# Performance work log

Hardware: AMD Instinct MI355X
Metric: run time of the kernel (lower is better)

The kernel has to match this reference:

```python
import jax, jax.numpy as jnp
import numpy as np

EPS = 1e-12  # torch F.normalize eps

def _colnorm(w, g):
    # F.normalize(w, dim=0, p=2) * g  (column-wise L2 over dim 0)
    n = jnp.sqrt(jnp.sum(w * w, axis=0, keepdims=True))
    return (w / jnp.maximum(n, EPS)) * g

def setup_inputs() -> dict:
    key = jax.random.key(0)
    ks = jax.random.split(key, 16)
    B, T, V, E, H = 16, 512, 8192, 512, 1024
    inp = {
        'xs': jax.random.randint(ks[0], (B, T), 0, V),
        'ys': jax.random.randint(ks[1], (B, T), 0, V),
        'embed_w': jax.random.normal(ks[2], (V, E), jnp.float32) * 0.02,
        'wx': jax.random.normal(ks[3], (E, 4 * H), jnp.float32),
        'wh': jax.random.normal(ks[4], (H, 4 * H), jnp.float32),
        'wmx': jax.random.normal(ks[5], (E, H), jnp.float32),
        'wmh': jax.random.normal(ks[6], (H, H), jnp.float32),
        'b': jax.random.normal(ks[7], (4 * H,), jnp.float32) * 0.02,
        'gx': jax.random.normal(ks[8], (4 * H,), jnp.float32),
        'gh': jax.random.normal(ks[9], (4 * H,), jnp.float32),
        'gmx': jax.random.normal(ks[10], (H,), jnp.float32),
        'gmh': jax.random.normal(ks[11], (H,), jnp.float32),
        'pred_w': jax.random.normal(ks[12], (V, H), jnp.float32) * 0.02,
        'pred_b': jax.random.normal(ks[13], (V,), jnp.float32) * 0.02,
    }
    return inp

def reference(xs, ys, embed_w, wx, wh, wmx, wmh, b, gx, gh, gmx, gmh, pred_w, pred_b):
    B, T = xs.shape
    H = wmh.shape[0]
    V = pred_w.shape[0]
    # padding_idx=0 -> embedding row 0 is zero
    ew = embed_w.at[0].set(0.0)
    x = ew[xs]  # [B, T, E]
    # weight norm
    wx_n = _colnorm(wx, gx)
    wh_n = _colnorm(wh, gh)
    wmx_n = _colnorm(wmx, gmx)
    wmh_n = _colnorm(wmh, gmh)
    # precompute input-dependent projections (same math, batched over time)
    zx = jnp.einsum('bte,ef->btf', x, wx_n) + b     # [B, T, 4H]
    mx = jnp.einsum('bte,eh->bth', x, wmx_n)        # [B, T, H]

    def step(carry, inp):
        h, c = carry
        zx_t, mx_t = inp
        m = mx_t * (h @ wmh_n)                       # [B, H]
        z = zx_t + m @ wh_n                          # [B, 4H]
        i, f, o, u = jnp.split(z, 4, axis=1)
        i = jax.nn.sigmoid(i)
        f = jax.nn.sigmoid(f)
        o = jax.nn.sigmoid(o)
        u = jnp.tanh(u)
        c = f * c + i * u
        h = o * jnp.tanh(c)
        return (h, c), h

    h0 = jnp.zeros((B, H), x.dtype)
    c0 = jnp.zeros((B, H), x.dtype)
    _, hs = jax.lax.scan(step, (h0, c0), (zx.transpose(1, 0, 2), mx.transpose(1, 0, 2)))
    hs = hs.transpose(1, 0, 2)  # [B, T, H]
    logits = jnp.einsum('bth,vh->btv', hs, pred_w) + pred_b
    log_p = jax.nn.log_softmax(logits.reshape(B * T, V), axis=-1)
    nll = -jnp.take_along_axis(log_p, ys.reshape(B * T, 1), axis=1)
    return jnp.mean(nll)
```

## Files before the change

### kernel.cpp

```cpp
#include <hip/hip_runtime.h>
#include <hip/hip_bf16.h>
#include <stdint.h>

#define B_   16
#define T_   512
#define V_   8192
#define E_   512
#define H_   1024
#define BT_  (B_ * T_)
#define H4_  (4 * H_)

typedef __attribute__((ext_vector_type(8))) short   short8;
typedef __attribute__((ext_vector_type(8))) __bf16  bf16x8;
typedef __attribute__((ext_vector_type(4))) float   f32x4;
typedef __attribute__((ext_vector_type(4))) short   short4v;
typedef unsigned long long ull;

__device__ __forceinline__ float bf2f(short s) {
  union { unsigned u; float f; } x;
  x.u = ((unsigned)(unsigned short)s) << 16;
  return x.f;
}
__device__ __forceinline__ short f2bf(float f) {
  union { float f; unsigned u; } x; x.f = f;
  unsigned u = x.u;
  u = (u + 0x7fffu + ((u >> 16) & 1u)) >> 16;
  return (short)u;
}
__device__ __forceinline__ f32x4 mfma16(short8 a, short8 b, f32x4 c) {
  return __builtin_amdgcn_mfma_f32_16x16x32_bf16(
      __builtin_bit_cast(bf16x8, a), __builtin_bit_cast(bf16x8, b), c, 0, 0, 0);
}
__device__ __forceinline__ float sigm(float x) { return 1.f / (1.f + __expf(-x)); }
__device__ __forceinline__ float tanh_f(float x) { return 1.f - 2.f / (__expf(2.f * x) + 1.f); }

__device__ __forceinline__ short8 mk8(ull lo, ull hi) {
  union { ull u[2]; short8 s; } c;
  c.u[0] = lo; c.u[1] = hi;
  return c.s;
}

__global__ __launch_bounds__(256) void colscale(const float* __restrict__ W,
                                                const float* __restrict__ g,
                                                float* __restrict__ sc, int Kr, int N) {
  int j = blockIdx.x * 256 + threadIdx.x;
  if (j >= N) return;
  float ss = 0.f;
  for (int i = 0; i < Kr; ++i) { float v = W[(long)i * N + j]; ss = fmaf(v, v, ss); }
  sc[j] = g[j] / fmaxf(sqrtf(ss), 1e-12f);
}

__global__ __launch_bounds__(256) void transpose_cast(const float* __restrict__ W,
                                                      const float* __restrict__ sc,
                                                      short* __restrict__ WT, int Kr, int N) {
  __shared__ float tile[32][33];
  int nbi = Kr >> 5;
  int bi = blockIdx.x % nbi, bj = blockIdx.x / nbi;
  int i0 = bi << 5, j0 = bj << 5;
  int tx = threadIdx.x & 31, ty = threadIdx.x >> 5;
  for (int yy = ty; yy < 32; yy += 8)
    tile[yy][tx] = W[(long)(i0 + yy) * N + j0 + tx];
  __syncthreads();
  for (int yy = ty; yy < 32; yy += 8) {
    int j = j0 + yy;
    WT[(long)j * Kr + i0 + tx] = f2bf(tile[tx][yy] * sc[j]);
  }
}

__global__ __launch_bounds__(256) void castbf(const float* __restrict__ src,
                                              short* __restrict__ dst, long n) {
  long i = ((long)blockIdx.x * 256 + threadIdx.x) * 4;
  if (i + 3 < n) {
    float4 v = *(const float4*)(src + i);
    short4v o = { f2bf(v.x), f2bf(v.y), f2bf(v.z), f2bf(v.w) };
    *(short4v*)(dst + i) = o;
  }
}

__global__ __launch_bounds__(256) void embed_gather(const int* __restrict__ xs,
                                                    const float* __restrict__ ew,
                                                    short* __restrict__ x) {
  int r = blockIdx.x;
  int idx = xs[r];
  const float* src = ew + (long)idx * E_;
  for (int e = threadIdx.x; e < E_; e += 256) {
    float v = (idx == 0) ? 0.f : src[e];
    x[(long)r * E_ + e] = f2bf(v);
  }
}

__global__ __launch_bounds__(256) void gemm_bt(const short* __restrict__ A,
                                               const short* __restrict__ BT,
                                               const float* __restrict__ bias,
                                               short* __restrict__ C,
                                               int M, int N, int K) {
  int ntiles = N >> 7;
  int tM = (blockIdx.x / ntiles) << 7;
  int tN = (blockIdx.x % ntiles) << 7;
  int w = threadIdx.x >> 6, lane = threadIdx.x & 63;
  int mo = tM + ((w & 1) << 6), no = tN + ((w >> 1) << 6);
  int lr = lane & 15, lk8 = (lane >> 4) << 3, q = lane >> 4;
  f32x4 acc[4][4] = {};
  const short* Ap = A + (long)(mo + lr) * K + lk8;
  const short* Bp = BT + (long)(no + lr) * K + lk8;
  for (int k0 = 0; k0 < K; k0 += 32) {
    short8 af[4], bfr[4];
#pragma unroll
    for (int i = 0; i < 4; ++i) af[i] = *(const short8*)(Ap + (long)16 * i * K + k0);
#pragma unroll
    for (int j = 0; j < 4; ++j) bfr[j] = *(const short8*)(Bp + (long)16 * j * K + k0);
#pragma unroll
    for (int i = 0; i < 4; ++i)
#pragma unroll
      for (int j = 0; j < 4; ++j)
        acc[i][j] = mfma16(af[i], bfr[j], acc[i][j]);
  }
  float pbv[4];
#pragma unroll
  for (int j = 0; j < 4; ++j) pbv[j] = bias ? bias[no + 16 * j + lr] : 0.f;
#pragma unroll
  for (int i = 0; i < 4; ++i)
#pragma unroll
    for (int j = 0; j < 4; ++j)
#pragma unroll
      for (int r = 0; r < 4; ++r) {
        int row = mo + 16 * i + 4 * q + r;
        int col = no + 16 * j + lr;
        C[(long)row * N + col] = f2bf(acc[i][j][r] + pbv[j]);
      }
}

__global__ __launch_bounds__(256) void gemm_logits(const short* __restrict__ A,
                                                   const short* __restrict__ BT,
                                                   const float* __restrict__ pb,
                                                   const int* __restrict__ ys,
                                                   float* __restrict__ sumexp,
                                                   float* __restrict__ logit_y,
                                                   int M, int N, int K) {
  int ntiles = N >> 7;
  int tM = (blockIdx.x / ntiles) << 7;
  int tN = (blockIdx.x % ntiles) << 7;
  int w = threadIdx.x >> 6, lane = threadIdx.x & 63;
  int mo = tM + ((w & 1) << 6), no = tN + ((w >> 1) << 6);
  int lr = lane & 15, lk8 = (lane >> 4) << 3, q = lane >> 4;
  f32x4 acc[4][4] = {};
  const short* Ap = A + (long)(mo + lr) * K + lk8;
  const short* Bp = BT + (long)(no + lr) * K + lk8;
  for (int k0 = 0; k0 < K; k0 += 32) {
    short8 af[4], bfr[4];
#pragma unroll
    for (int i = 0; i < 4; ++i) af[i] = *(const short8*)(Ap + (long)16 * i * K + k0);
#pragma unroll
    for (int j = 0; j < 4; ++j) bfr[j] = *(const short8*)(Bp + (long)16 * j * K + k0);
#pragma unroll
    for (int i = 0; i < 4; ++i)
#pragma unroll
      for (int j = 0; j < 4; ++j)
        acc[i][j] = mfma16(af[i], bfr[j], acc[i][j]);
  }
  float pbv[4];
#pragma unroll
  for (int j = 0; j < 4; ++j) pbv[j] = pb[no + 16 * j + lr];
#pragma unroll
  for (int i = 0; i < 4; ++i) {
#pragma unroll
    for (int r = 0; r < 4; ++r) {
      int row = mo + 16 * i + 4 * q + r;
      int ysr = ys[row];
      float s = 0.f;
#pragma unroll
      for (int j = 0; j < 4; ++j) {
        float v = acc[i][j][r] + pbv[j];
        s += __expf(v);
        int col = no + 16 * j + lr;
        if (col == ysr) logit_y[row] = v;
      }
      s += __shfl_xor(s, 1); s += __shfl_xor(s, 2);
      s += __shfl_xor(s, 4); s += __shfl_xor(s, 8);
      if (lr == 0) atomicAdd(&sumexp[row], s);
    }
  }
}

#define NWG_ 64

__global__ __launch_bounds__(256, 1) void scan_kernel(
    const short* __restrict__ zxb, const short* __restrict__ mxb,
    const short* __restrict__ wmhT, const short* __restrict__ whT,
    short* __restrict__ hs,
    ull* __restrict__ h_ex,
    ull* __restrict__ m_ex,
    unsigned* __restrict__ flags_m,
    unsigned* __restrict__ flags_h) {
  const int g = blockIdx.x;
  const int tid = threadIdx.x;
  const int w = tid >> 6, lane = tid & 63;
  const int lr = lane & 15, q = lane >> 4;
  const int colg = g << 4;
  const int b = tid >> 4, cl = tid & 15;

  __shared__ float red1[4][16][16];
  __shared__ float red2[4][4][16][16];

  short8 wmh_f[8];
#pragma unroll
  for (int kk = 0; kk < 8; ++kk) {
    const ull* p = (const ull*)(wmhT + (long)(colg + lr) * H_ + (w << 8) + (kk << 5) + (q << 3));
    ull lo = __hip_atomic_load(p, __ATOMIC_RELAXED, __HIP_MEMORY_SCOPE_WORKGROUP);
    ull hi = __hip_atomic_load(p + 1, __ATOMIC_RELAXED, __HIP_MEMORY_SCOPE_WORKGROUP);
    wmh_f[kk] = mk8(lo, hi);
  }
  short8 wh_f[4][8];
#pragma unroll
  for (int gt = 0; gt < 4; ++gt)
#pragma unroll
    for (int kk = 0; kk < 8; ++kk) {
      const ull* p = (const ull*)(whT + (long)(gt * H_ + colg + lr) * H_ + (w << 8) + (kk << 5) + (q << 3));
      ull lo = __hip_atomic_load(p, __ATOMIC_RELAXED, __HIP_MEMORY_SCOPE_WORKGROUP);
      ull hi = __hip_atomic_load(p + 1, __ATOMIC_RELAXED, __HIP_MEMORY_SCOPE_WORKGROUP);
      wh_f[gt][kk] = mk8(lo, hi);
    }

  float c = 0.f;
  const ull* hp = h_ex + lr * 256 + (w << 6) + (q << 1);
  const ull* mp = m_ex + lr * 256 + (w << 6) + (q << 1);
  const unsigned* fh_poll = flags_h + (((w << 4) + (lane >> 2)) * 4 + (lane & 3)) * 16;
  const unsigned* fm_poll = flags_m + ((w << 4) + lr) * 16;
  const int b2 = tid >> 2, ch = tid & 3;
  ull* m_st = m_ex + (b2 << 8) + (colg >> 2) + ch;
  unsigned* h_st = (unsigned*)h_ex + (((b << 10) + colg + cl) >> 1);

  for (int t = 0; t < T_; ++t) {
    long rrow = (long)(b * T_ + t);
    const short* zrow = zxb + rrow * H4_ + colg + cl;
    short z0p = zrow[0 * H_], z1p = zrow[1 * H_], z2p = zrow[2 * H_], z3p = zrow[3 * H_];
    ull mxq = 0;
    if (w == 0)
      mxq = *(const ull*)(mxb + (long)(b2 * T_ + t) * H_ + colg + (ch << 2));

    while (__hip_atomic_load(fh_poll, __ATOMIC_RELAXED, __HIP_MEMORY_SCOPE_AGENT)
           < (unsigned)t) {}

    ull lh[16];
#pragma unroll
    for (int kk = 0; kk < 8; ++kk) {
      lh[2 * kk]     = __hip_atomic_load(hp + (kk << 3),     __ATOMIC_RELAXED, __HIP_MEMORY_SCOPE_AGENT);
      lh[2 * kk + 1] = __hip_atomic_load(hp + (kk << 3) + 1, __ATOMIC_RELAXED, __HIP_MEMORY_SCOPE_AGENT);
    }
    f32x4 a1 = {};
#pragma unroll
    for (int kk = 0; kk < 8; ++kk)
      a1 = mfma16(mk8(lh[2 * kk], lh[2 * kk + 1]), wmh_f[kk], a1);
#pragma unroll
    for (int r = 0; r < 4; ++r) red1[w][q * 4 + r][lr] = a1[r];
    __syncthreads();

    if (w == 0) {
      union { short4v s; ull u; } pk;
      union { short4v s; ull u; } mxu; mxu.u = mxq;
#pragma unroll
      for (int u = 0; u < 4; ++u) {
        float s = red1[0][b2][(ch << 2) + u] + red1[1][b2][(ch << 2) + u] +
                  red1[2][b2][(ch << 2) + u] + red1[3][b2][(ch << 2) + u];
        pk.s[u] = f2bf(bf2f(mxu.s[u]) * s);
      }
      __hip_atomic_store(m_st, pk.u, __ATOMIC_RELAXED, __HIP_MEMORY_SCOPE_AGENT);
      __builtin_amdgcn_s_waitcnt(0);
      if (tid == 0)
        __hip_atomic_store(&flags_m[g << 4], (unsigned)(t + 1),
                           __ATOMIC_RELAXED, __HIP_MEMORY_SCOPE_AGENT);
    }

    while (__hip_atomic_load(fm_poll, __ATOMIC_RELAXED, __HIP_MEMORY_SCOPE_AGENT)
           < (unsigned)(t + 1)) {}

    ull lm[16];
#pragma unroll
    for (int kk = 0; kk < 8; ++kk) {
      lm[2 * kk]     = __hip_atomic_load(mp + (kk << 3),     __ATOMIC_RELAXED, __HIP_MEMORY_SCOPE_AGENT);
      lm[2 * kk + 1] = __hip_atomic_load(mp + (kk << 3) + 1, __ATOMIC_RELAXED, __HIP_MEMORY_SCOPE_AGENT);
    }
    f32x4 a2[4] = {};
#pragma unroll
    for (int kk = 0; kk < 8; ++kk) {
      short8 mf = mk8(lm[2 * kk], lm[2 * kk + 1]);
#pragma unroll
      for (int gt = 0; gt < 4; ++gt)
        a2[gt] = mfma16(mf, wh_f[gt][kk], a2[gt]);
    }
#pragma unroll
    for (int gt = 0; gt < 4; ++gt)
#pragma unroll
      for (int r = 0; r < 4; ++r)
        red2[w][gt][q * 4 + r][lr] = a2[gt][r];
    __syncthreads();

    {
      float zi = red2[0][0][b][cl] + red2[1][0][b][cl] + red2[2][0][b][cl] + red2[3][0][b][cl] + bf2f(z0p);
      float zf = red2[0][1][b][cl] + red2[1][1][b][cl] + red2[2][1][b][cl] + red2[3][1][b][cl] + bf2f(z1p);
      float zo = red2[0][2][b][cl] + red2[1][2][b][cl] + red2[2][2][b][cl] + red2[3][2][b][cl] + bf2f(z2p);
      float zu = red2[0][3][b][cl] + red2[1][3][b][cl] + red2[2][3][b][cl] + red2[3][3][b][cl] + bf2f(z3p);
      float ig = sigm(zi), fg = sigm(zf), og = sigm(zo), ug = tanh_f(zu);
      c = fg * c + ig * ug;
      float h = og * tanh_f(c);
      short hb = f2bf(h);
      hs[rrow * H_ + colg + cl] = hb;
      unsigned hv = (unsigned)(unsigned short)hb;
      unsigned ov = (unsigned)__shfl_xor((int)hv, 1);
      if ((lane & 1) == 0)
        __hip_atomic_store(h_st, hv | (ov << 16),
                           __ATOMIC_RELAXED, __HIP_MEMORY_SCOPE_AGENT);
      __builtin_amdgcn_s_waitcnt(0);
      if (lane == 0)
        __hip_atomic_store(&flags_h[((g << 2) + w) << 4], (unsigned)(t + 1),
                           __ATOMIC_RELAXED, __HIP_MEMORY_SCOPE_AGENT);
    }
  }
}

__global__ __launch_bounds__(256) void reduce_nll(const float* __restrict__ se,
                                                  const float* __restrict__ ly,
                                                  float* __restrict__ out) {
  __shared__ float buf[256];
  float s = 0.f;
  for (int r = threadIdx.x; r < BT_; r += 256)
    s += logf(se[r]) - ly[r];
  buf[threadIdx.x] = s;
  __syncthreads();
  for (int off = 128; off > 0; off >>= 1) {
    if (threadIdx.x < off) buf[threadIdx.x] += buf[threadIdx.x + off];
    __syncthreads();
  }
  if (threadIdx.x == 0) out[0] = buf[0] * (1.0f / BT_);
}

extern "C" void kernel_launch(void* const* d_in, const int* in_sizes, int n_in,
                              void* d_out, int out_size, void* d_ws, size_t ws_size,
                              hipStream_t stream) {
  const int*   xs     = (const int*)d_in[0];
  const int*   ys     = (const int*)d_in[1];
  const float* embw   = (const float*)d_in[2];
  const float* wx     = (const float*)d_in[3];
  const float* wh     = (const float*)d_in[4];
  const float* wmx    = (const float*)d_in[5];
  const float* wmh    = (const float*)d_in[6];
  const float* bias   = (const float*)d_in[7];
  const float* gx     = (const float*)d_in[8];
  const float* gh     = (const float*)d_in[9];
  const float* gmx    = (const float*)d_in[10];
  const float* gmh    = (const float*)d_in[11];
  const float* pred_w = (const float*)d_in[12];
  const float* pred_b = (const float*)d_in[13];
  float* out = (float*)d_out;

  char* base = (char*)d_ws;
  size_t off = 0;
  auto alloc = [&](size_t bytes) -> void* {
    void* p = base + off;
    off = (off + bytes + 255) & ~(size_t)255;
    return p;
  };
  short* xb     = (short*)alloc((size_t)BT_ * E_ * 2);
  short* zxb    = (short*)alloc((size_t)BT_ * H4_ * 2);
  short* mxb    = (short*)alloc((size_t)BT_ * H_ * 2);
  short* hs     = (short*)alloc((size_t)BT_ * H_ * 2);
  short* wxT    = (short*)alloc((size_t)H4_ * E_ * 2);
  short* whT    = (short*)alloc((size_t)H4_ * H_ * 2);
  short* wmxT   = (short*)alloc((size_t)H_ * E_ * 2);
  short* wmhT   = (short*)alloc((size_t)H_ * H_ * 2);
  short* pwb    = (short*)alloc((size_t)V_ * H_ * 2);
  float* scx    = (float*)alloc(H4_ * 4);
  float* sch    = (float*)alloc(H4_ * 4);
  float* scmx   = (float*)alloc(H_ * 4);
  float* scmh   = (float*)alloc(H_ * 4);
  float* l_y    = (float*)alloc(BT_ * 4);
  ull*   m_ex   = (ull*)alloc((size_t)B_ * H_ * 2);
  size_t z0 = off;
  float*    sumexp  = (float*)alloc(BT_ * 4);
  unsigned* flags_m = (unsigned*)alloc(NWG_ * 16 * 4);
  unsigned* flags_h = (unsigned*)alloc(NWG_ * 4 * 16 * 4);
  ull*      h_ex    = (ull*)alloc((size_t)B_ * H_ * 2);
  size_t zlen = off - z0;

  hipMemsetAsync(base + z0, 0, zlen, stream);

  colscale<<<H4_ / 256, 256, 0, stream>>>(wx, gx, scx, E_, H4_);
  colscale<<<H4_ / 256, 256, 0, stream>>>(wh, gh, sch, H_, H4_);
  colscale<<<H_ / 256, 256, 0, stream>>>(wmx, gmx, scmx, E_, H_);
  colscale<<<H_ / 256, 256, 0, stream>>>(wmh, gmh, scmh, H_, H_);
  transpose_cast<<<(E_ / 32) * (H4_ / 32), 256, 0, stream>>>(wx, scx, wxT, E_, H4_);
  transpose_cast<<<(H_ / 32) * (H4_ / 32), 256, 0, stream>>>(wh, sch, whT, H_, H4_);
  transpose_cast<<<(E_ / 32) * (H_ / 32), 256, 0, stream>>>(wmx, scmx, wmxT, E_, H_);
  transpose_cast<<<(H_ / 32) * (H_ / 32), 256, 0, stream>>>(wmh, scmh, wmhT, H_, H_);
  castbf<<<((long)V_ * H_) / 1024, 256, 0, stream>>>(pred_w, pwb, (long)V_ * H_);

  embed_gather<<<BT_, 256, 0, stream>>>(xs, embw, xb);
  gemm_bt<<<(BT_ / 128) * (H4_ / 128), 256, 0, stream>>>(xb, wxT, bias, zxb, BT_, H4_, E_);
  gemm_bt<<<(BT_ / 128) * (H_ / 128), 256, 0, stream>>>(xb, wmxT, nullptr, mxb, BT_, H_, E_);

  scan_kernel<<<NWG_, 256, 0, stream>>>(zxb, mxb, wmhT, whT, hs,
                                        h_ex, m_ex, flags_m, flags_h);

  gemm_logits<<<(BT_ / 128) * (V_ / 128), 256, 0, stream>>>(hs, pwb, pred_b, ys,
                                                            sumexp, l_y, BT_, V_, H_);
  reduce_nll<<<1, 256, 0, stream>>>(sumexp, l_y, out);
}
```

Before: 5.862 ms.

## Fuse logits GEMM into scan kernel to overlap with recurrence

Merges the recurrent scan and the logits/softmax GEMM into one launch. 64 blocks run the scan and 192 extra blocks wait on per-wave progress counters, then compute logits tiles for each completed 128-timestep chunk. The aim is to hide logits GEMM time behind the latency-bound sequential scan. The logits blocks read hs with atomic loads and poll progress flags, which may add contention and relies on all 256 blocks being co-resident.

```diff
diff --git a/kernel.cpp b/kernel.cpp
--- a/kernel.cpp
+++ b/kernel.cpp
@@ -130,190 +130,217 @@
       }
 }
 
-__global__ __launch_bounds__(256) void gemm_logits(const short* __restrict__ A,
-                                                   const short* __restrict__ BT,
-                                                   const float* __restrict__ pb,
-                                                   const int* __restrict__ ys,
-                                                   float* __restrict__ sumexp,
-                                                   float* __restrict__ logit_y,
-                                                   int M, int N, int K) {
-  int ntiles = N >> 7;
-  int tM = (blockIdx.x / ntiles) << 7;
-  int tN = (blockIdx.x % ntiles) << 7;
-  int w = threadIdx.x >> 6, lane = threadIdx.x & 63;
-  int mo = tM + ((w & 1) << 6), no = tN + ((w >> 1) << 6);
-  int lr = lane & 15, lk8 = (lane >> 4) << 3, q = lane >> 4;
-  f32x4 acc[4][4] = {};
-  const short* Ap = A + (long)(mo + lr) * K + lk8;
-  const short* Bp = BT + (long)(no + lr) * K + lk8;
-  for (int k0 = 0; k0 < K; k0 += 32) {
-    short8 af[4], bfr[4];
-#pragma unroll
-    for (int i = 0; i < 4; ++i) af[i] = *(const short8*)(Ap + (long)16 * i * K + k0);
-#pragma unroll
-    for (int j = 0; j < 4; ++j) bfr[j] = *(const short8*)(Bp + (long)16 * j * K + k0);
-#pragma unroll
-    for (int i = 0; i < 4; ++i)
-#pragma unroll
-      for (int j = 0; j < 4; ++j)
-        acc[i][j] = mfma16(af[i], bfr[j], acc[i][j]);
-  }
-  float pbv[4];
-#pragma unroll
-  for (int j = 0; j < 4; ++j) pbv[j] = pb[no + 16 * j + lr];
-#pragma unroll
-  for (int i = 0; i < 4; ++i) {
-#pragma unroll
-    for (int r = 0; r < 4; ++r) {
-      int row = mo + 16 * i + 4 * q + r;
-      int ysr = ys[row];
-      float s = 0.f;
-#pragma unroll
-      for (int j = 0; j < 4; ++j) {
-        float v = acc[i][j][r] + pbv[j];
-        s += __expf(v);
-        int col = no + 16 * j + lr;
-        if (col == ysr) logit_y[row] = v;
-      }
-      s += __shfl_xor(s, 1); s += __shfl_xor(s, 2);
-      s += __shfl_xor(s, 4); s += __shfl_xor(s, 8);
-      if (lr == 0) atomicAdd(&sumexp[row], s);
-    }
-  }
-}
-
-#define NWG_ 64
-
-__global__ __launch_bounds__(256, 1) void scan_kernel(
+#define NWG_  64
+#define NLOG_ 192
+
+__global__ __launch_bounds__(256, 1) void scan_logits(
     const short* __restrict__ zxb, const short* __restrict__ mxb,
     const short* __restrict__ wmhT, const short* __restrict__ whT,
     short* __restrict__ hs,
     ull* __restrict__ h_ex,
     ull* __restrict__ m_ex,
     unsigned* __restrict__ flags_m,
-    unsigned* __restrict__ flags_h) {
-  const int g = blockIdx.x;
+    unsigned* __restrict__ flags_h,
+    unsigned* __restrict__ prog,
+    const short* __restrict__ pwb,
+    const float* __restrict__ pb,
+    const int* __restrict__ ys,
+    float* __restrict__ sumexp,
+    float* __restrict__ logit_y) {
+  const int blk = blockIdx.x;
   const int tid = threadIdx.x;
   const int w = tid >> 6, lane = tid & 63;
   const int lr = lane & 15, q = lane >> 4;
-  const int colg = g << 4;
-  const int b = tid >> 4, cl = tid & 15;
-
-  __shared__ float red1[4][16][16];
-  __shared__ float red2[4][4][16][16];
-
-  short8 wmh_f[8];
-#pragma unroll
-  for (int kk = 0; kk < 8; ++kk) {
-    const ull* p = (const ull*)(wmhT + (long)(colg + lr) * H_ + (w << 8) + (kk << 5) + (q << 3));
-    ull lo = __hip_atomic_load(p, __ATOMIC_RELAXED, __HIP_MEMORY_SCOPE_WORKGROUP);
-    ull hi = __hip_atomic_load(p + 1, __ATOMIC_RELAXED, __HIP_MEMORY_SCOPE_WORKGROUP);
-    wmh_f[kk] = mk8(lo, hi);
-  }
-  short8 wh_f[4][8];
-#pragma unroll
-  for (int gt = 0; gt < 4; ++gt)
+
+  if (blk < NWG_) {
+    const int g = blk;
+    const int colg = g << 4;
+    const int b = tid >> 4, cl = tid & 15;
+
+    __shared__ float red1[4][16][16];
+    __shared__ float red2[4][4][16][16];
+
+    short8 wmh_f[8];
 #pragma unroll
     for (int kk = 0; kk < 8; ++kk) {
-      const ull* p = (const ull*)(whT + (long)(gt * H_ + colg + lr) * H_ + (w << 8) + (kk << 5) + (q << 3));
+      const ull* p = (const ull*)(wmhT + (long)(colg + lr) * H_ + (w << 8) + (kk << 5) + (q << 3));
       ull lo = __hip_atomic_load(p, __ATOMIC_RELAXED, __HIP_MEMORY_SCOPE_WORKGROUP);
       ull hi = __hip_atomic_load(p + 1, __ATOMIC_RELAXED, __HIP_MEMORY_SCOPE_WORKGROUP);
-      wh_f[gt][kk] = mk8(lo, hi);
+      wmh_f[kk] = mk8(lo, hi);
     }
-
-  float c = 0.f;
-  const ull* hp = h_ex + lr * 256 + (w << 6) + (q << 1);
-  const ull* mp = m_ex + lr * 256 + (w << 6) + (q << 1);
-  const unsigned* fh_poll = flags_h + (((w << 4) + (lane >> 2)) * 4 + (lane & 3)) * 16;
-  const unsigned* fm_poll = flags_m + ((w << 4) + lr) * 16;
-  const int b2 = tid >> 2, ch = tid & 3;
-  ull* m_st = m_ex + (b2 << 8) + (colg >> 2) + ch;
-  unsigned* h_st = (unsigned*)h_ex + (((b << 10) + colg + cl) >> 1);
-
-  for (int t = 0; t < T_; ++t) {
-    long rrow = (long)(b * T_ + t);
-    const short* zrow = zxb + rrow * H4_ + colg + cl;
-    short z0p = zrow[0 * H_], z1p = zrow[1 * H_], z2p = zrow[2 * H_], z3p = zrow[3 * H_];
-    ull mxq = 0;
-    if (w == 0)
-      mxq = *(const ull*)(mxb + (long)(b2 * T_ + t) * H_ + colg + (ch << 2));
-
-    while (__hip_atomic_load(fh_poll, __ATOMIC_RELAXED, __HIP_MEMORY_SCOPE_AGENT)
-           < (unsigned)t) {}
-
-    ull lh[16];
-#pragma unroll
-    for (int kk = 0; kk < 8; ++kk) {
-      lh[2 * kk]     = __hip_atomic_load(hp + (kk << 3),     __ATOMIC_RELAXED, __HIP_MEMORY_SCOPE_AGENT);
-      lh[2 * kk + 1] = __hip_atomic_load(hp + (kk << 3) + 1, __ATOMIC_RELAXED, __HIP_MEMORY_SCOPE_AGENT);
+    short8 wh_f[4][8];
+#pragma unroll
+    for (int gt = 0; gt < 4; ++gt)
+#pragma unroll
+      for (int kk = 0; kk < 8; ++kk) {
+        const ull* p = (const ull*)(whT + (long)(gt * H_ + colg + lr) * H_ + (w << 8) + (kk << 5) + (q << 3));
+        ull lo = __hip_atomic_load(p, __ATOMIC_RELAXED, __HIP_MEMORY_SCOPE_WORKGROUP);
+        ull hi = __hip_atomic_load(p + 1, __ATOMIC_RELAXED, __HIP_MEMORY_SCOPE_WORKGROUP);
+        wh_f[gt][kk] = mk8(lo, hi);
+      }
+
+    float c = 0.f;
+    const ull* hp = h_ex + lr * 256 + (w << 6) + (q << 1);
+    const ull* mp = m_ex + lr * 256 + (w << 6) + (q << 1);
+    const unsigned* fhp = flags_h + (((w << 4) + (lane >> 2)) * 4 + (lane & 3)) * 16;
+    const unsigned* fmp = flags_m + ((w << 4) + lr) * 16;
+    const int b2 = tid >> 2, ch = tid & 3;
+    ull* m_st = m_ex + (b2 << 8) + (colg >> 2) + ch;
+    unsigned* h_st = (unsigned*)h_ex + (((b << 10) + colg + cl) >> 1);
+
+    for (int t = 0; t < T_; ++t) {
+      long rrow = (long)(b * T_ + t);
+      const short* zrow = zxb + rrow * H4_ + colg + cl;
+      short z0p = zrow[0 * H_], z1p = zrow[1 * H_], z2p = zrow[2 * H_], z3p = zrow[3 * H_];
+      ull mxq = 0;
+      if (w == 0)
+        mxq = *(const ull*)(mxb + (long)(b2 * T_ + t) * H_ + colg + (ch << 2));
+
+      while (__hip_atomic_load(fhp, __ATOMIC_RELAXED, __HIP_MEMORY_SCOPE_AGENT)
+             < (unsigned)t) {}
+
+      ull lh[16];
+#pragma unroll
+      for (int kk = 0; kk < 8; ++kk) {
+        lh[2 * kk]     = __hip_atomic_load(hp + (kk << 3),     __ATOMIC_RELAXED, __HIP_MEMORY_SCOPE_AGENT);
+        lh[2 * kk + 1] = __hip_atomic_load(hp + (kk << 3) + 1, __ATOMIC_RELAXED, __HIP_MEMORY_SCOPE_AGENT);
+      }
+      f32x4 a1 = {};
+#pragma unroll
+      for (int kk = 0; kk < 8; ++kk)
+        a1 = mfma16(mk8(lh[2 * kk], lh[2 * kk + 1]), wmh_f[kk], a1);
+#pragma unroll
+      for (int r = 0; r < 4; ++r) red1[w][q * 4 + r][lr] = a1[r];
+      __syncthreads();
+
+      if (w == 0) {
+        union { short4v s; ull u; } pk;
+        union { short4v s; ull u; } mxu; mxu.u = mxq;
+#pragma unroll
+        for (int u = 0; u < 4; ++u) {
+          float s = red1[0][b2][(ch << 2) + u] + red1[1][b2][(ch << 2) + u] +
+                    red1[2][b2][(ch << 2) + u] + red1[3][b2][(ch << 2) + u];
+          pk.s[u] = f2bf(bf2f(mxu.s[u]) * s);
+        }
+        __hip_atomic_store(m_st, pk.u, __ATOMIC_RELAXED, __HIP_MEMORY_SCOPE_AGENT);
+        __builtin_amdgcn_s_waitcnt(0);
+        if (tid == 0)
+          __hip_atomic_store(&flags_m[g << 4], (unsigned)(t + 1),
+                             __ATOMIC_RELAXED, __HIP_MEMORY_SCOPE_AGENT);
+      }
+
+      while (__hip_atomic_load(fmp, __ATOMIC_RELAXED, __HIP_MEMORY_SCOPE_AGENT)
+             < (unsigned)(t + 1)) {}
+
+      ull lm[16];
+#pragma unroll
+      for (int kk = 0; kk < 8; ++kk) {
+        lm[2 * kk]     = __hip_atomic_load(mp + (kk << 3),     __ATOMIC_RELAXED, __HIP_MEMORY_SCOPE_AGENT);
+        lm[2 * kk + 1] = __hip_atomic_load(mp + (kk << 3) + 1, __ATOMIC_RELAXED, __HIP_MEMORY_SCOPE_AGENT);
+      }
+      f32x4 a2[4] = {};
+#pragma unroll
+      for (int kk = 0; kk < 8; ++kk) {
+        short8 mf = mk8(lm[2 * kk], lm[2 * kk + 1]);
+#pragma unroll
+        for (int gt = 0; gt < 4; ++gt)
+          a2[gt] = mfma16(mf, wh_f[gt][kk], a2[gt]);
+      }
+#pragma unroll
+      for (int gt = 0; gt < 4; ++gt)
+#pragma unroll
+        for (int r = 0; r < 4; ++r)
+          red2[w][gt][q * 4 + r][lr] = a2[gt][r];
+      __syncthreads();
+
+      {
+        float zi = red2[0][0][b][cl] + red2[1][0][b][cl] + red2[2][0][b][cl] + red2[3][0][b][cl] + bf2f(z0p);
+        float zf = red2[0][1][b][cl] + red2[1][1][b][cl] + red2[2][1][b][cl] + red2[3][1][b][cl] + bf2f(z1p);
+        float zo = red2[0][2][b][cl] + red2[1][2][b][cl] + red2[2][2][b][cl] + red2[3][2][b][cl] + bf2f(z2p);
+        float zu = red2[0][3][b][cl] + red2[1][3][b][cl] + red2[2][3][b][cl] + red2[3][3][b][cl] + bf2f(z3p);
+        float ig = sigm(zi), fg = sigm(zf), og = sigm(zo), ug = tanh_f(zu);
+        c = fg * c + ig * ug;
+        float h = og * tanh_f(c);
+        short hb = f2bf(h);
+        unsigned hv = (unsigned)(unsigned short)hb;
+        unsigned ov = (unsigned)__shfl_xor((int)hv, 1);
+        unsigned packed = hv | (ov << 16);
+        if ((lane & 1) == 0) {
+          __hip_atomic_store(h_st, packed, __ATOMIC_RELAXED, __HIP_MEMORY_SCOPE_AGENT);
+          __hip_atomic_store((unsigned*)hs + (((rrow << 10) + colg + cl) >> 1),
+                             packed, __ATOMIC_RELAXED, __HIP_MEMORY_SCOPE_AGENT);
+        }
+        __builtin_amdgcn_s_waitcnt(0);
+        if (lane == 0) {
+          __hip_atomic_store(&flags_h[((g << 2) + w) << 4], (unsigned)(t + 1),
+                             __ATOMIC_RELAXED, __HIP_MEMORY_SCOPE_AGENT);
+          __hip_atomic_store(&prog[(g << 2) + w], (unsigned)(t + 1),
+                             __ATOMIC_RELAXED, __HIP_MEMORY_SCOPE_AGENT);
+        }
+      }
     }
-    f32x4 a1 = {};
-#pragma unroll
-    for (int kk = 0; kk < 8; ++kk)
-      a1 = mfma16(mk8(lh[2 * kk], lh[2 * kk + 1]), wmh_f[kk], a1);
-#pragma unroll
-    for (int r = 0; r < 4; ++r) red1[w][q * 4 + r][lr] = a1[r];
-    __syncthreads();
-
-    if (w == 0) {
-      union { short4v s; ull u; } pk;
-      union { short4v s; ull u; } mxu; mxu.u = mxq;
-#pragma unroll
-      for (int u = 0; u < 4; ++u) {
-        float s = red1[0][b2][(ch << 2) + u] + red1[1][b2][(ch << 2) + u] +
-                  red1[2][b2][(ch << 2) + u] + red1[3][b2][(ch << 2) + u];
-        pk.s[u] = f2bf(bf2f(mxu.s[u]) * s);
-      }
-      __hip_atomic_store(m_st, pk.u, __ATOMIC_RELAXED, __HIP_MEMORY_SCOPE_AGENT);
-      __builtin_amdgcn_s_waitcnt(0);
-      if (tid == 0)
-        __hip_atomic_store(&flags_m[g << 4], (unsigned)(t + 1),
-                           __ATOMIC_RELAXED, __HIP_MEMORY_SCOPE_AGENT);
-    }
-
-    while (__hip_atomic_load(fm_poll, __ATOMIC_RELAXED, __HIP_MEMORY_SCOPE_AGENT)
-           < (unsigned)(t + 1)) {}
-
-    ull lm[16];
-#pragma unroll
-    for (int kk = 0; kk < 8; ++kk) {
-      lm[2 * kk]     = __hip_atomic_load(mp + (kk << 3),     __ATOMIC_RELAXED, __HIP_MEMORY_SCOPE_AGENT);
-      lm[2 * kk + 1] = __hip_atomic_load(mp + (kk << 3) + 1, __ATOMIC_RELAXED, __HIP_MEMORY_SCOPE_AGENT);
-    }
-    f32x4 a2[4] = {};
-#pragma unroll
-    for (int kk = 0; kk < 8; ++kk) {
-      short8 mf = mk8(lm[2 * kk], lm[2 * kk + 1]);
-#pragma unroll
-      for (int gt = 0; gt < 4; ++gt)
-        a2[gt] = mfma16(mf, wh_f[gt][kk], a2[gt]);
-    }
-#pragma unroll
-    for (int gt = 0; gt < 4; ++gt)
-#pragma unroll
-      for (int r = 0; r < 4; ++r)
-        red2[w][gt][q * 4 + r][lr] = a2[gt][r];
-    __syncthreads();
-
-    {
-      float zi = red2[0][0][b][cl] + red2[1][0][b][cl] + red2[2][0][b][cl] + red2[3][0][b][cl] + bf2f(z0p);
-      float zf = red2[0][1][b][cl] + red2[1][1][b][cl] + red2[2][1][b][cl] + red2[3][1][b][cl] + bf2f(z1p);
-      float zo = red2[0][2][b][cl] + red2[1][2][b][cl] + red2[2][2][b][cl] + red2[3][2][b][cl] + bf2f(z2p);
-      float zu = red2[0][3][b][cl] + red2[1][3][b][cl] + red2[2][3][b][cl] + red2[3][3][b][cl] + bf2f(z3p);
-      float ig = sigm(zi), fg = sigm(zf), og = sigm(zo), ug = tanh_f(zu);
-      c = fg * c + ig * ug;
-      float h = og * tanh_f(c);
-      short hb = f2bf(h);
-      hs[rrow * H_ + colg + cl] = hb;
-      unsigned hv = (unsigned)(unsigned short)hb;
-      unsigned ov = (unsigned)__shfl_xor((int)hv, 1);
-      if ((lane & 1) == 0)
-        __hip_atomic_store(h_st, hv | (ov << 16),
-                           __ATOMIC_RELAXED, __HIP_MEMORY_SCOPE_AGENT);
-      __builtin_amdgcn_s_waitcnt(0);
-      if (lane == 0)
-        __hip_atomic_store(&flags_h[((g << 2) + w) << 4], (unsigned)(t + 1),
-                           __ATOMIC_RELAXED, __HIP_MEMORY_SCOPE_AGENT);
+  } else {
+    const int wid = blk - NWG_;
+    const int lk8 = (lane >> 4) << 3;
+    int lastp = -1;
+    for (int s = wid; s < (BT_ / 128) * (V_ / 128); s += NLOG_) {
+      const int p = s >> 10;
+      const int rem = s & 1023;
+      const int bb = rem >> 6, vb = rem & 63;
+      if (p != lastp) {
+        const unsigned target = (unsigned)((p + 1) << 7);
+        const unsigned* pp = prog + tid;
+        while (__hip_atomic_load(pp, __ATOMIC_RELAXED, __HIP_MEMORY_SCOPE_AGENT)
+               < target)
+          __builtin_amdgcn_s_sleep(127);
+        __syncthreads();
+        lastp = p;
+      }
+      const int tM = ((bb << 2) + p) << 7;
+      const int tN = vb << 7;
+      const int mo = tM + ((w & 1) << 6), no = tN + ((w >> 1) << 6);
+      f32x4 acc[4][4] = {};
+      const ull* Ap = (const ull*)hs + (((long)(mo + lr) << 10) + lk8 >> 2);
+      const short* Bp = pwb + (long)(no + lr) * H_ + lk8;
+      for (int k0 = 0; k0 < H_; k0 += 32) {
+        short8 af[4], bfr[4];
+#pragma unroll
+        for (int i = 0; i < 4; ++i) {
+          const ull* pa = Ap + (long)i * 4096 + (k0 >> 2);
+          ull lo = __hip_atomic_load(pa,     __ATOMIC_RELAXED, __HIP_MEMORY_SCOPE_AGENT);
+          ull hi = __hip_atomic_load(pa + 1, __ATOMIC_RELAXED, __HIP_MEMORY_SCOPE_AGENT);
+          af[i] = mk8(lo, hi);
+        }
+#pragma unroll
+        for (int j = 0; j < 4; ++j) bfr[j] = *(const short8*)(Bp + (long)16 * j * H_ + k0);
+#pragma unroll
+        for (int i = 0; i < 4; ++i)
+#pragma unroll
+          for (int j = 0; j < 4; ++j)
+            acc[i][j] = mfma16(af[i], bfr[j], acc[i][j]);
+      }
+      float pbv[4];
+#pragma unroll
+      for (int j = 0; j < 4; ++j) pbv[j] = pb[no + 16 * j + lr];
+#pragma unroll
+      for (int i = 0; i < 4; ++i) {
+#pragma unroll
+        for (int r = 0; r < 4; ++r) {
+          int row = mo + 16 * i + 4 * q + r;
+          int ysr = ys[row];
+          float sum = 0.f;
+#pragma unroll
+          for (int j = 0; j < 4; ++j) {
+            float v = acc[i][j][r] + pbv[j];
+            sum += __expf(v);
+            int col = no + 16 * j + lr;
+            if (col == ysr) logit_y[row] = v;
+          }
+          sum += __shfl_xor(sum, 1); sum += __shfl_xor(sum, 2);
+          sum += __shfl_xor(sum, 4); sum += __shfl_xor(sum, 8);
+          if (lr == 0) atomicAdd(&sumexp[row], sum);
+        }
+      }
     }
   }
 }
@@ -379,6 +406,7 @@
   float*    sumexp  = (float*)alloc(BT_ * 4);
   unsigned* flags_m = (unsigned*)alloc(NWG_ * 16 * 4);
   unsigned* flags_h = (unsigned*)alloc(NWG_ * 4 * 16 * 4);
+  unsigned* prog    = (unsigned*)alloc(NWG_ * 4 * 4);
   ull*      h_ex    = (ull*)alloc((size_t)B_ * H_ * 2);
   size_t zlen = off - z0;
 
@@ -398,10 +426,9 @@
   gemm_bt<<<(BT_ / 128) * (H4_ / 128), 256, 0, stream>>>(xb, wxT, bias, zxb, BT_, H4_, E_);
   gemm_bt<<<(BT_ / 128) * (H_ / 128), 256, 0, stream>>>(xb, wmxT, nullptr, mxb, BT_, H_, E_);
 
-  scan_kernel<<<NWG_, 256, 0, stream>>>(zxb, mxb, wmhT, whT, hs,
-                                        h_ex, m_ex, flags_m, flags_h);
-
-  gemm_logits<<<(BT_ / 128) * (V_ / 128), 256, 0, stream>>>(hs, pwb, pred_b, ys,
-                                                            sumexp, l_y, BT_, V_, H_);
+  scan_logits<<<NWG_ + NLOG_, 256, 0, stream>>>(zxb, mxb, wmhT, whT, hs,
+                                                h_ex, m_ex, flags_m, flags_h, prog,
+                                                pwb, pred_b, ys, sumexp, l_y);
+
   reduce_nll<<<1, 256, 0, stream>>>(sumexp, l_y, out);
 }
```

Result: slower. 6.046 ms (+3.1%).
